# Kernel tuning notes

Hardware: AMD Instinct MI355X
Metric: run time of the kernel (lower is better)

## Reference

```python
import jax, jax.numpy as jnp
import numpy as np

N_NODES = 100000
N_EDGES = 1600000
NODE_DIM = 128
HIDDEN = 128
OUT_DIM = 128
N_GRAPHS = 64
LN_EPS = 1e-5


def setup_inputs() -> dict:
    key = jax.random.key(0)
    ks = jax.random.split(key, 14)

    def lin(k, fan_in, fan_out):
        bound = 1.0 / np.sqrt(fan_in)
        kw, kb = jax.random.split(k)
        W = jax.random.uniform(kw, (fan_in, fan_out), jnp.float32, -bound, bound)
        b = jax.random.uniform(kb, (fan_out,), jnp.float32, -bound, bound)
        return W, b

    node_features = jax.random.normal(ks[0], (N_NODES, NODE_DIM), jnp.float32)
    edge_index = jax.random.randint(ks[1], (2, N_EDGES), 0, N_NODES, jnp.int32)
    batch = jnp.sort(jax.random.randint(ks[2], (N_NODES,), 0, N_GRAPHS, jnp.int32))

    W1, b1 = lin(ks[3], NODE_DIM, HIDDEN)
    W2, b2 = lin(ks[4], HIDDEN, HIDDEN)
    W3, b3 = lin(ks[5], HIDDEN, OUT_DIM)
    Wm1, bm1 = lin(ks[6], OUT_DIM, HIDDEN)
    Wm2, bm2 = lin(ks[7], HIDDEN, OUT_DIM)
    ln_g = jnp.ones((OUT_DIM,), jnp.float32)
    ln_b = jnp.zeros((OUT_DIM,), jnp.float32)

    return dict(node_features=node_features, edge_index=edge_index, batch=batch,
                W1=W1, b1=b1, W2=W2, b2=b2, W3=W3, b3=b3,
                Wm1=Wm1, bm1=bm1, Wm2=Wm2, bm2=bm2, ln_g=ln_g, ln_b=ln_b)


def _gcn_precompute(edge_index, n_nodes):
    # Add self-loops; symmetric degree normalization (PyG GCNConv semantics).
    loops = jnp.arange(n_nodes, dtype=edge_index.dtype)
    src = jnp.concatenate([edge_index[0], loops])
    dst = jnp.concatenate([edge_index[1], loops])
    deg = jax.ops.segment_sum(jnp.ones_like(dst, jnp.float32), dst, num_segments=n_nodes)
    dinv = jax.lax.rsqrt(deg)  # deg >= 1 thanks to self-loops
    norm = dinv[src] * dinv[dst]  # [E + N]
    return src, dst, norm


def _gcn_layer(x, W, b, src, dst, norm, n_nodes):
    xw = x @ W                              # [N, F_out]
    msg = norm[:, None] * xw[src]           # [E+N, F_out] gather
    agg = jax.ops.segment_sum(msg, dst, num_segments=n_nodes)  # scatter-add
    return agg + b


def reference(node_features, edge_index, batch,
              W1, b1, W2, b2, W3, b3, Wm1, bm1, Wm2, bm2, ln_g, ln_b):
    n_nodes = node_features.shape[0]
    src, dst, norm = _gcn_precompute(edge_index, n_nodes)

    x = jax.nn.relu(_gcn_layer(node_features, W1, b1, src, dst, norm, n_nodes))
    x = jax.nn.relu(_gcn_layer(x, W2, b2, src, dst, norm, n_nodes))
    x = _gcn_layer(x, W3, b3, src, dst, norm, n_nodes)  # no relu on last layer

    # global mean pool per graph
    sums = jax.ops.segment_sum(x, batch, num_segments=N_GRAPHS)
    cnts = jax.ops.segment_sum(jnp.ones((n_nodes,), x.dtype), batch, num_segments=N_GRAPHS)
    g = sums / jnp.maximum(cnts, 1.0)[:, None]  # [G, OUT_DIM]

    # global reasoner MLP + LayerNorm
    h = jax.nn.relu(g @ Wm1 + bm1)
    y = h @ Wm2 + bm2
    mu = jnp.mean(y, axis=-1, keepdims=True)
    var = jnp.var(y, axis=-1, keepdims=True)
    y = (y - mu) * jax.lax.rsqrt(var + LN_EPS) * ln_g + ln_b
    return y
```

## Files before the change

### kernel.cpp

```cpp
#include <hip/hip_runtime.h>

#define FDIM 128
#define LN_EPS 1e-5f
#define NBKT_SHIFT 8
#define BKT_NODES 256
#define MAXBKT 512
#define CAP_SHIFT 13
#define BKT_CAP 8192

typedef short bf16x8 __attribute__((ext_vector_type(8)));
typedef float f32x4 __attribute__((ext_vector_type(4)));
typedef float f32x2 __attribute__((ext_vector_type(2)));
typedef ushort u16x8 __attribute__((ext_vector_type(8)));
typedef unsigned long long u64;
typedef long long i64;

static __device__ __forceinline__ ushort f2bf(float f) {
    union { float f; unsigned u; } v; v.f = f;
    unsigned r = v.u + 0x7FFFu + ((v.u >> 16) & 1u);
    return (ushort)(r >> 16);
}
static __device__ __forceinline__ float bf2f(ushort h) {
    union { unsigned u; float f; } v; v.u = ((unsigned)h) << 16;
    return v.f;
}
static __device__ __forceinline__ unsigned char f2fp8(float f) {
    return (unsigned char)__builtin_amdgcn_cvt_pk_fp8_f32(f, f, 0u, false);
}
static __device__ __forceinline__ float fp8tof(unsigned char b) {
    f32x2 p = __builtin_amdgcn_cvt_pk_f32_fp8((unsigned)b, false);
    return p[0];
}
static __device__ __forceinline__ void fp8x8_add(uint2 w, f32x2* acc) {
    acc[0] += __builtin_amdgcn_cvt_pk_f32_fp8(w.x, false);
    acc[1] += __builtin_amdgcn_cvt_pk_f32_fp8(w.x, true);
    acc[2] += __builtin_amdgcn_cvt_pk_f32_fp8(w.y, false);
    acc[3] += __builtin_amdgcn_cvt_pk_f32_fp8(w.y, true);
}


__launch_bounds__(256)
__global__ void k_bkt_scatter(const int* __restrict__ src, const int* __restrict__ dst,
                              int* __restrict__ bcur, unsigned* __restrict__ bktA,
                              int E, int nbkt) {
    __shared__ int h[2][MAXBKT], lbase[2][MAXBKT], lcur[2][MAXBKT];
    const int t = threadIdx.x;
    const int half = t >> 7;
    for (int i = t; i < 2 * MAXBKT; i += 256) ((int*)h)[i] = 0;
    __syncthreads();
    const int E4 = E >> 2;
    const int4* s4p = (const int4*)src;
    const int4* d4p = (const int4*)dst;
    int4 sv[4], dv[4]; bool ok[4];
#pragma unroll
    for (int r = 0; r < 4; r++) {
        int i4 = blockIdx.x * 1024 + r * 256 + t;
        ok[r] = (i4 < E4);
        if (ok[r]) {
            sv[r] = s4p[i4]; dv[r] = d4p[i4];
            atomicAdd(&h[half][dv[r].x >> NBKT_SHIFT], 1);
            atomicAdd(&h[half][dv[r].y >> NBKT_SHIFT], 1);
            atomicAdd(&h[half][dv[r].z >> NBKT_SHIFT], 1);
            atomicAdd(&h[half][dv[r].w >> NBKT_SHIFT], 1);
        }
    }
    __syncthreads();
    for (int i = t; i < 2 * nbkt; i += 256) {
        const int hh = (i >= nbkt) ? 1 : 0;
        const int b = hh ? (i - nbkt) : i;
        const int c = h[hh][b];
        lbase[hh][b] = c ? ((b << CAP_SHIFT) + atomicAdd(&bcur[b], c)) : 0;
        lcur[hh][b] = 0;
    }
    __syncthreads();
#pragma unroll
    for (int r = 0; r < 4; r++) {
        if (!ok[r]) continue;
        int ss[4] = {sv[r].x, sv[r].y, sv[r].z, sv[r].w};
        int dd[4] = {dv[r].x, dv[r].y, dv[r].z, dv[r].w};
#pragma unroll
        for (int j = 0; j < 4; j++) {
            int b = dd[j] >> NBKT_SHIFT;
            int p = atomicAdd(&lcur[half][b], 1);
            bktA[(size_t)lbase[half][b] + p] =
                ((unsigned)ss[j] << NBKT_SHIFT) | (unsigned)(dd[j] & (BKT_NODES - 1));
        }
    }
}


__launch_bounds__(512)
__global__ void k_build(const unsigned* __restrict__ bktA, const int* __restrict__ bcur,
                        int2* __restrict__ rowinfo, float* __restrict__ dinv,
                        int* __restrict__ csr_src, int N) {
    __shared__ int sorted[BKT_CAP];
    __shared__ int cnt[BKT_NODES];
    __shared__ int cur[BKT_NODES];
    __shared__ int wpart[4], wbase[4];
    const int t = threadIdx.x;
    const int b = blockIdx.x;
    const int nb = b << NBKT_SHIFT;
    if (t < BKT_NODES) cnt[t] = 0;
    __syncthreads();
    const int beg = b << CAP_SHIFT;
    const int tot = bcur[b];
    for (int i = t; i < tot; i += 512)
        atomicAdd(&cnt[bktA[beg + i] & (BKT_NODES - 1)], 1);
    __syncthreads();
    const int lane = t & 63, wv = t >> 6;
    int my = 0, x = 0;
    if (t < BKT_NODES) {
        my = cnt[t];
        x = my;
#pragma unroll
        for (int off = 1; off < 64; off <<= 1) {
            int y = __shfl_up(x, off, 64);
            if (lane >= off) x += y;
        }
        if (lane == 63) wpart[wv] = x;
    }
    __syncthreads();
    if (t == 0) {
        int s = 0;
        for (int w = 0; w < 4; w++) { int tmp = wpart[w]; wbase[w] = s; s += tmp; }
    }
    __syncthreads();
    if (t < BKT_NODES) {
        const int incl = x + wbase[wv];
        const int rbeg = incl - my;
        cur[t] = rbeg;
        const int n = nb + t;
        if (n < N) {
            rowinfo[n] = make_int2(beg + rbeg, my);
            dinv[n] = rsqrtf((float)(my + 1));
        }
    }
    __syncthreads();
    for (int i = t; i < tot; i += 512) {
        unsigned pr = bktA[beg + i];
        int d = pr & (BKT_NODES - 1);
        int p = atomicAdd(&cur[d], 1);
        sorted[p] = (int)(pr >> NBKT_SHIFT);
    }
    __syncthreads();
    for (int i = t; i < tot; i += 512)
        csr_src[beg + i] = sorted[i];
}


__global__ void k_prep_w(const float* __restrict__ Wa, const float* __restrict__ Wb,
                         const float* __restrict__ Wc, ushort* __restrict__ Wt_b,
                         unsigned char* __restrict__ Wt8, float* __restrict__ gsums,
                         int* __restrict__ bcur) {
    int idx = blockIdx.x * 256 + threadIdx.x;
    int layer = idx >> 14;
    int r = idx & 16383;
    int nn = r >> 7, kk = r & 127;
    if (layer == 0) {
        Wt_b[r] = f2bf(Wa[kk * 128 + nn]);
    } else {
        const float* W = (layer == 1) ? Wb : Wc;
        Wt8[(size_t)(layer - 1) * 16384 + r] = f2fp8(W[kk * 128 + nn]);
    }
    if (idx < 8192) gsums[idx] = 0.f;
    if (idx < MAXBKT) bcur[idx] = 0;
}


__launch_bounds__(256)
__global__ void k_gemm_f32(const float* __restrict__ X, const ushort* __restrict__ Wt,
                           const float* __restrict__ dinv, unsigned char* __restrict__ C,
                           int N) {
    __shared__ __align__(16) ushort As[128][136];
    __shared__ ushort Ws[128][136];
    const int t = threadIdx.x;
    const int row0 = blockIdx.x * 128;

#pragma unroll
    for (int i = 0; i < 8; i++) {
        int c = t + i * 256;
        int r = c >> 4, c8 = (c & 15) * 8;
        *(bf16x8*)&Ws[r][c8] = *(const bf16x8*)&Wt[r * 128 + c8];
    }
#pragma unroll
    for (int i = 0; i < 8; i++) {
        int c = t + i * 256;
        int r = c >> 4, c8 = (c & 15) * 8;
        int row = row0 + r;
        bf16x8 pk = {0, 0, 0, 0, 0, 0, 0, 0};
        if (row < N) {
            const float* sp = X + (size_t)row * FDIM + c8;
            float4 u0 = *(const float4*)(sp);
            float4 u1 = *(const float4*)(sp + 4);
            pk[0] = (short)f2bf(u0.x); pk[1] = (short)f2bf(u0.y);
            pk[2] = (short)f2bf(u0.z); pk[3] = (short)f2bf(u0.w);
            pk[4] = (short)f2bf(u1.x); pk[5] = (short)f2bf(u1.y);
            pk[6] = (short)f2bf(u1.z); pk[7] = (short)f2bf(u1.w);
        }
        *(bf16x8*)&As[r][c8] = pk;
    }
    __syncthreads();

    const int w = t >> 6, l = t & 63;
    const int m = l & 15, q = l >> 4;
    const int r0 = w * 32;

    bf16x8 a0[4], a1[4];
#pragma unroll
    for (int ks = 0; ks < 4; ks++) {
        a0[ks] = *(const bf16x8*)&As[r0 + m][ks * 32 + q * 8];
        a1[ks] = *(const bf16x8*)&As[r0 + 16 + m][ks * 32 + q * 8];
    }

    f32x4 acc0[8], acc1[8];
#pragma unroll
    for (int ct = 0; ct < 8; ct++) { acc0[ct] = {0, 0, 0, 0}; acc1[ct] = {0, 0, 0, 0}; }

#pragma unroll
    for (int ct = 0; ct < 8; ct++) {
#pragma unroll
        for (int ks = 0; ks < 4; ks++) {
            bf16x8 b = *(const bf16x8*)&Ws[ct * 16 + m][ks * 32 + q * 8];
            acc0[ct] = __builtin_amdgcn_mfma_f32_16x16x32_bf16(a0[ks], b, acc0[ct], 0, 0, 0);
            acc1[ct] = __builtin_amdgcn_mfma_f32_16x16x32_bf16(a1[ks], b, acc1[ct], 0, 0, 0);
        }
    }

    float dv0[4], dv1[4];
#pragma unroll
    for (int r = 0; r < 4; r++) {
        int row = row0 + r0 + q * 4 + r;
        dv0[r] = (row < N) ? dinv[row] : 0.f;
        dv1[r] = (row + 16 < N) ? dinv[row + 16] : 0.f;
    }

    __syncthreads();
    char* Ab = (char*)&As[0][0];
#pragma unroll
    for (int ct = 0; ct < 8; ct++) {
#pragma unroll
        for (int r = 0; r < 4; r++) {
            int rl = r0 + q * 4 + r;
            Ab[rl * 128 + ct * 16 + m] = (char)f2fp8(acc0[ct][r] * dv0[r]);
            Ab[(rl + 16) * 128 + ct * 16 + m] = (char)f2fp8(acc1[ct][r] * dv1[r]);
        }
    }
    __syncthreads();
    const uint4* As4 = (const uint4*)Ab;
#pragma unroll
    for (int i = 0; i < 4; i++) {
        int c = t + i * 256;
        int row = c >> 3;
        int col = (c & 7) * 16;
        int grow = row0 + row;
        if (grow < N) *(uint4*)&C[(size_t)grow * FDIM + col] = As4[c];
    }
}


__launch_bounds__(256)
__global__ void k_gemm_fp8(const unsigned char* __restrict__ X,
                           const unsigned char* __restrict__ W8,
                           const float* __restrict__ dinv, unsigned char* __restrict__ C,
                           int N) {
    __shared__ __align__(16) unsigned char As[128][144];
    __shared__ __align__(16) unsigned char Ws[128][144];
    const int t = threadIdx.x;
    const int row0 = blockIdx.x * 128;

#pragma unroll
    for (int i = 0; i < 4; i++) {
        int c = t + i * 256;
        int r = c >> 3, col = (c & 7) * 16;
        *(uint4*)&Ws[r][col] = *(const uint4*)&W8[r * 128 + col];
        int row = row0 + r;
        uint4 v = {0, 0, 0, 0};
        if (row < N) v = *(const uint4*)&X[(size_t)row * FDIM + col];
        *(uint4*)&As[r][col] = v;
    }
    __syncthreads();

    const int w = t >> 6, l = t & 63;
    const int m = l & 15, q = l >> 4;
    const int r0 = w * 32;

    i64 a0[4], a1[4];
#pragma unroll
    for (int ks = 0; ks < 4; ks++) {
        a0[ks] = *(const i64*)&As[r0 + m][ks * 32 + q * 8];
        a1[ks] = *(const i64*)&As[r0 + 16 + m][ks * 32 + q * 8];
    }

    f32x4 acc0[8], acc1[8];
#pragma unroll
    for (int ct = 0; ct < 8; ct++) { acc0[ct] = {0, 0, 0, 0}; acc1[ct] = {0, 0, 0, 0}; }

#pragma unroll
    for (int ct = 0; ct < 8; ct++) {
#pragma unroll
        for (int ks = 0; ks < 4; ks++) {
            i64 b = *(const i64*)&Ws[ct * 16 + m][ks * 32 + q * 8];
            acc0[ct] = __builtin_amdgcn_mfma_f32_16x16x32_fp8_fp8(a0[ks], b, acc0[ct], 0, 0, 0);
            acc1[ct] = __builtin_amdgcn_mfma_f32_16x16x32_fp8_fp8(a1[ks], b, acc1[ct], 0, 0, 0);
        }
    }

    float dv0[4], dv1[4];
#pragma unroll
    for (int r = 0; r < 4; r++) {
        int row = row0 + r0 + q * 4 + r;
        dv0[r] = (row < N) ? dinv[row] : 0.f;
        dv1[r] = (row + 16 < N) ? dinv[row + 16] : 0.f;
    }

    __syncthreads();
    char* Ab = (char*)&As[0][0];
#pragma unroll
    for (int ct = 0; ct < 8; ct++) {
#pragma unroll
        for (int r = 0; r < 4; r++) {
            int rl = r0 + q * 4 + r;
            Ab[rl * 128 + ct * 16 + m] = (char)f2fp8(acc0[ct][r] * dv0[r]);
            Ab[(rl + 16) * 128 + ct * 16 + m] = (char)f2fp8(acc1[ct][r] * dv1[r]);
        }
    }
    __syncthreads();
    const uint4* As4 = (const uint4*)Ab;
#pragma unroll
    for (int i = 0; i < 4; i++) {
        int c = t + i * 256;
        int row = c >> 3;
        int col = (c & 7) * 16;
        int grow = row0 + row;
        if (grow < N) *(uint4*)&C[(size_t)grow * FDIM + col] = As4[c];
    }
}


__launch_bounds__(256)
__global__ void k_aggregate(const unsigned char* __restrict__ xs8,
                            const int2* __restrict__ rowinfo,
                            const int* __restrict__ csr_src, const float* __restrict__ dinv,
                            const float* __restrict__ bias, unsigned char* __restrict__ out,
                            int N, int do_relu) {
    const int n = (blockIdx.x << 2) + (threadIdx.x >> 6);
    if (n >= N) return;
    const int l = threadIdx.x & 63;
    const int fl = l & 15;
    const int grp = l >> 4;
    const unsigned foff = (unsigned)fl << 3;

    f32x2 acc[4] = {{0, 0}, {0, 0}, {0, 0}, {0, 0}};
    if (grp == 0) {
        uint2 sv = *(const uint2*)(xs8 + (((unsigned)n << 7) | foff));
        fp8x8_add(sv, acc);
    }

    const int2 ri = rowinfo[n];
    const int beg = ri.x;
    const int deg = ri.y;

    for (int base = 0; base < deg; base += 64) {
        const int m = min(64, deg - base);
        int idx = 0;
        if (l < m) idx = csr_src[(unsigned)(beg + base + l)];
        int j = grp;
        if (j < m) {
            int s0 = __shfl(idx, j, 64);
            uint2 v0 = *(const uint2*)(xs8 + (((unsigned)s0 << 7) | foff));
            int j2 = j + 4;
            if (j2 < m) {
                int s1 = __shfl(idx, j2, 64);
                uint2 v1 = *(const uint2*)(xs8 + (((unsigned)s1 << 7) | foff));
                for (j = j2 + 4; j < m; j += 4) {
                    int s2 = __shfl(idx, j, 64);
                    uint2 v2 = *(const uint2*)(xs8 + (((unsigned)s2 << 7) | foff));
                    fp8x8_add(v0, acc);
                    v0 = v1; v1 = v2;
                }
                fp8x8_add(v0, acc);
                fp8x8_add(v1, acc);
            } else {
                fp8x8_add(v0, acc);
            }
        }
    }

    float a[8] = {acc[0][0], acc[0][1], acc[1][0], acc[1][1],
                  acc[2][0], acc[2][1], acc[3][0], acc[3][1]};
#pragma unroll
    for (int k = 0; k < 8; k++) {
        a[k] += __shfl_xor(a[k], 16, 64);
        a[k] += __shfl_xor(a[k], 32, 64);
    }

    if (grp == 0) {
        const float d = dinv[n];
        const float4 b0 = ((const float4*)bias)[fl * 2];
        const float4 b1 = ((const float4*)bias)[fl * 2 + 1];
        const float bb[8] = {b0.x, b0.y, b0.z, b0.w, b1.x, b1.y, b1.z, b1.w};
        float v[8];
#pragma unroll
        for (int k = 0; k < 8; k++) {
            v[k] = d * a[k] + bb[k];
            if (do_relu) v[k] = fmaxf(v[k], 0.f);
        }
        uint2 o;
        unsigned d0 = __builtin_amdgcn_cvt_pk_fp8_f32(v[0], v[1], 0u, false);
        o.x = __builtin_amdgcn_cvt_pk_fp8_f32(v[2], v[3], d0, true);
        unsigned d1 = __builtin_amdgcn_cvt_pk_fp8_f32(v[4], v[5], 0u, false);
        o.y = __builtin_amdgcn_cvt_pk_fp8_f32(v[6], v[7], d1, true);
        ((uint2*)out)[(size_t)n * 16 + fl] = o;
    }
}


__launch_bounds__(256)
__global__ void k_pool(const unsigned char* __restrict__ x3, const int* __restrict__ batch,
                       float* __restrict__ sums, int N) {
    const int t = threadIdx.x;
    const int fq = t & 31;
    const int sub = t >> 5;
    const int n0 = blockIdx.x * 256 + sub * 32;
    if (n0 >= N) return;
    const int n1 = (n0 + 32 < N) ? n0 + 32 : N;

    f32x4 acc = {0.f, 0.f, 0.f, 0.f};
    int cur = batch[n0];
    for (int n = n0; n < n1; n++) {
        int g = batch[n];
        if (g != cur) {
            float* s = &sums[cur * FDIM + (fq << 2)];
            atomicAdd(s + 0, acc[0]); atomicAdd(s + 1, acc[1]);
            atomicAdd(s + 2, acc[2]); atomicAdd(s + 3, acc[3]);
            acc = (f32x4){0.f, 0.f, 0.f, 0.f};
            cur = g;
        }
        unsigned w = *(const unsigned*)(x3 + ((size_t)n << 7) + (fq << 2));
        f32x2 lo = __builtin_amdgcn_cvt_pk_f32_fp8(w, false);
        f32x2 hi = __builtin_amdgcn_cvt_pk_f32_fp8(w, true);
        acc[0] += lo[0]; acc[1] += lo[1]; acc[2] += hi[0]; acc[3] += hi[1];
    }
    float* s = &sums[cur * FDIM + (fq << 2)];
    atomicAdd(s + 0, acc[0]); atomicAdd(s + 1, acc[1]);
    atomicAdd(s + 2, acc[2]); atomicAdd(s + 3, acc[3]);
}


__launch_bounds__(128)
__global__ void k_final(const float* __restrict__ sums, const int* __restrict__ batch, int N,
                        const float* __restrict__ Wm1, const float* __restrict__ bm1,
                        const float* __restrict__ Wm2, const float* __restrict__ bm2,
                        const float* __restrict__ ln_g, const float* __restrict__ ln_b,
                        float* __restrict__ out) {
    const int g = blockIdx.x;
    const int t = threadIdx.x;

    int lo = 0, hi = N;
    while (lo < hi) { int mid = (lo + hi) >> 1; if (batch[mid] < g) lo = mid + 1; else hi = mid; }
    int lo2 = lo, hi2 = N;
    while (lo2 < hi2) { int mid = (lo2 + hi2) >> 1; if (batch[mid] < g + 1) lo2 = mid + 1; else hi2 = mid; }
    float cnt = (float)(lo2 - lo);

    float gl = sums[g * FDIM + t] / fmaxf(cnt, 1.0f);

    __shared__ float gbuf[FDIM];
    __shared__ float hbuf[FDIM];
    __shared__ float wsum[4];
    gbuf[t] = gl;
    __syncthreads();

    float h = bm1[t];
#pragma unroll 8
    for (int k = 0; k < FDIM; k++) h += gbuf[k] * Wm1[k * FDIM + t];
    h = fmaxf(h, 0.f);
    hbuf[t] = h;
    __syncthreads();

    float y = bm2[t];
#pragma unroll 8
    for (int k = 0; k < FDIM; k++) y += hbuf[k] * Wm2[k * FDIM + t];

    float s = y, s2 = y * y;
#pragma unroll
    for (int off = 32; off > 0; off >>= 1) {
        s += __shfl_down(s, off, 64);
        s2 += __shfl_down(s2, off, 64);
    }
    if ((t & 63) == 0) { wsum[t >> 6] = s; wsum[2 + (t >> 6)] = s2; }
    __syncthreads();
    float sum = wsum[0] + wsum[1];
    float sumsq = wsum[2] + wsum[3];
    float mu = sum * (1.0f / FDIM);
    float var = sumsq * (1.0f / FDIM) - mu * mu;
    float r = rsqrtf(var + LN_EPS);
    out[g * FDIM + t] = (y - mu) * r * ln_g[t] + ln_b[t];
}


extern "C" void kernel_launch(void* const* d_in, const int* in_sizes, int n_in,
                              void* d_out, int out_size, void* d_ws, size_t ws_size,
                              hipStream_t stream) {
    const float* x_in  = (const float*)d_in[0];
    const int*   eidx  = (const int*)d_in[1];
    const int*   batch = (const int*)d_in[2];
    const float* W1 = (const float*)d_in[3];
    const float* b1 = (const float*)d_in[4];
    const float* W2 = (const float*)d_in[5];
    const float* b2 = (const float*)d_in[6];
    const float* W3 = (const float*)d_in[7];
    const float* b3 = (const float*)d_in[8];
    const float* Wm1 = (const float*)d_in[9];
    const float* bm1 = (const float*)d_in[10];
    const float* Wm2 = (const float*)d_in[11];
    const float* bm2 = (const float*)d_in[12];
    const float* ln_g = (const float*)d_in[13];
    const float* ln_b = (const float*)d_in[14];
    float* out = (float*)d_out;

    const int N = in_sizes[0] / FDIM;
    const int E = in_sizes[1] / 2;
    const int G = out_size / FDIM;

    const int* src = eidx;
    const int* dst = eidx + E;

    const int nbkt = (N + BKT_NODES - 1) >> NBKT_SHIFT;

    char* p = (char*)d_ws;
    unsigned* bktA = (unsigned*)p;    p += (size_t)nbkt * BKT_CAP * 4;
    unsigned char* B0q = (unsigned char*)p; p += (size_t)N * FDIM;
    unsigned char* B1q = (unsigned char*)p; p += (size_t)N * FDIM;
    int* csr_src = (int*)p;           p += (size_t)nbkt * BKT_CAP * 4;
    int2* rowinfo = (int2*)p;         p += (size_t)N * 8;
    float* dinv = (float*)p;          p += (size_t)N * 4;
    ushort* Wt_b = (ushort*)p;        p += 16384 * 2;
    unsigned char* Wt8 = (unsigned char*)p; p += 2 * 16384;
    float* gsums = (float*)p;         p += (size_t)G * FDIM * 4;
    int* bcur = (int*)p;              p += MAXBKT * 4;

    const int TPB = 256;
    dim3 blk(TPB);
    dim3 gAgg((N + 3) / 4);
    dim3 gTile((N + 127) / 128);
    const int nEb = (E + 4095) / 4096;

    k_prep_w<<<dim3(192), blk, 0, stream>>>(W1, W2, W3, Wt_b, Wt8, gsums, bcur);
    k_bkt_scatter<<<dim3(nEb), blk, 0, stream>>>(src, dst, bcur, bktA, E, nbkt);
    k_build<<<dim3(nbkt), dim3(512), 0, stream>>>(bktA, bcur, rowinfo, dinv, csr_src, N);

    k_gemm_f32<<<gTile, blk, 0, stream>>>(x_in, Wt_b, dinv, B0q, N);
    k_aggregate<<<gAgg, blk, 0, stream>>>(B0q, rowinfo, csr_src, dinv, b1, B1q, N, 1);

    k_gemm_fp8<<<gTile, blk, 0, stream>>>(B1q, Wt8, dinv, B0q, N);
    k_aggregate<<<gAgg, blk, 0, stream>>>(B0q, rowinfo, csr_src, dinv, b2, B1q, N, 1);

    k_gemm_fp8<<<gTile, blk, 0, stream>>>(B1q, Wt8 + 16384, dinv, B0q, N);
    k_aggregate<<<gAgg, blk, 0, stream>>>(B0q, rowinfo, csr_src, dinv, b3, B1q, N, 0);

    k_pool<<<dim3((N + 255) / 256), blk, 0, stream>>>(B1q, batch, gsums, N);
    k_final<<<dim3(G), dim3(FDIM), 0, stream>>>(gsums, batch, N, Wm1, bm1, Wm2, bm2,
                                                ln_g, ln_b, out);
}
```

Baseline: 384.4 us.

## Use half-wave per node in aggregation and fuse mean-pool into last layer

The aggregation kernel now assigns 32 lanes per node (8 nodes per block) instead of 64, with a deeper three-stage gather pipeline and a single cross-lane reduction. The final layer's aggregation accumulates pooled sums directly, via shared-memory atomics when a block's nodes share one graph and global atomics otherwise, which removes the separate pool kernel and the fp8 write and re-read of the last layer's output. The cost is more work per lane for high-degree nodes and global atomic contention in blocks that span a graph boundary. Pooling also now sums values before fp8 rounding, which slightly changes the numerics.

```diff
diff --git a/kernel.cpp b/kernel.cpp
--- a/kernel.cpp
+++ b/kernel.cpp
@@ -342,44 +342,68 @@
                             const int2* __restrict__ rowinfo,
                             const int* __restrict__ csr_src, const float* __restrict__ dinv,
                             const float* __restrict__ bias, unsigned char* __restrict__ out,
-                            int N, int do_relu) {
-    const int n = (blockIdx.x << 2) + (threadIdx.x >> 6);
-    if (n >= N) return;
-    const int l = threadIdx.x & 63;
-    const int fl = l & 15;
-    const int grp = l >> 4;
+                            const int* __restrict__ batch, float* __restrict__ gsums,
+                            int N, int do_relu, int fuse_pool) {
+    __shared__ float gsum_s[FDIM];
+    __shared__ int gb_s[8];
+    const int t = threadIdx.x;
+    const int l = t & 63;
+    const int node_slot = t >> 5;
+    const int n = blockIdx.x * 8 + node_slot;
+    const bool active = (n < N);
+    const int hl = l & 31;
+    const int fl = hl & 15;
+    const int grp = hl >> 4;
+    const int selbase = l & 32;
     const unsigned foff = (unsigned)fl << 3;
 
+    if (fuse_pool) {
+        if (t < FDIM) gsum_s[t] = 0.f;
+        if (t < 8) {
+            int nn = blockIdx.x * 8 + t;
+            gb_s[t] = batch[nn < N ? nn : (N - 1)];
+        }
+        __syncthreads();
+    }
+
     f32x2 acc[4] = {{0, 0}, {0, 0}, {0, 0}, {0, 0}};
-    if (grp == 0) {
+    int2 ri = active ? rowinfo[n] : make_int2(0, 0);
+    if (active && grp == 0) {
         uint2 sv = *(const uint2*)(xs8 + (((unsigned)n << 7) | foff));
         fp8x8_add(sv, acc);
     }
-
-    const int2 ri = rowinfo[n];
     const int beg = ri.x;
     const int deg = ri.y;
 
-    for (int base = 0; base < deg; base += 64) {
-        const int m = min(64, deg - base);
+    for (int base = 0; base < deg; base += 32) {
+        const int m = min(32, deg - base);
         int idx = 0;
-        if (l < m) idx = csr_src[(unsigned)(beg + base + l)];
+        if (hl < m) idx = csr_src[(unsigned)(beg + base + hl)];
         int j = grp;
         if (j < m) {
-            int s0 = __shfl(idx, j, 64);
+            int s0 = __shfl(idx, selbase | j, 64);
             uint2 v0 = *(const uint2*)(xs8 + (((unsigned)s0 << 7) | foff));
-            int j2 = j + 4;
-            if (j2 < m) {
-                int s1 = __shfl(idx, j2, 64);
+            int j1 = j + 2;
+            if (j1 < m) {
+                int s1 = __shfl(idx, selbase | j1, 64);
                 uint2 v1 = *(const uint2*)(xs8 + (((unsigned)s1 << 7) | foff));
-                for (j = j2 + 4; j < m; j += 4) {
-                    int s2 = __shfl(idx, j, 64);
+                int j2 = j1 + 2;
+                if (j2 < m) {
+                    int s2 = __shfl(idx, selbase | j2, 64);
                     uint2 v2 = *(const uint2*)(xs8 + (((unsigned)s2 << 7) | foff));
+                    for (j = j2 + 2; j < m; j += 2) {
+                        int s3 = __shfl(idx, selbase | j, 64);
+                        uint2 v3 = *(const uint2*)(xs8 + (((unsigned)s3 << 7) | foff));
+                        fp8x8_add(v0, acc);
+                        v0 = v1; v1 = v2; v2 = v3;
+                    }
                     fp8x8_add(v0, acc);
-                    v0 = v1; v1 = v2;
+                    fp8x8_add(v1, acc);
+                    fp8x8_add(v2, acc);
+                } else {
+                    fp8x8_add(v0, acc);
+                    fp8x8_add(v1, acc);
                 }
-                fp8x8_add(v0, acc);
-                fp8x8_add(v1, acc);
             } else {
                 fp8x8_add(v0, acc);
             }
@@ -389,12 +413,9 @@
     float a[8] = {acc[0][0], acc[0][1], acc[1][0], acc[1][1],
                   acc[2][0], acc[2][1], acc[3][0], acc[3][1]};
 #pragma unroll
-    for (int k = 0; k < 8; k++) {
-        a[k] += __shfl_xor(a[k], 16, 64);
-        a[k] += __shfl_xor(a[k], 32, 64);
-    }
-
-    if (grp == 0) {
+    for (int k = 0; k < 8; k++) a[k] += __shfl_xor(a[k], 16, 64);
+
+    if (active && grp == 0) {
         const float d = dinv[n];
         const float4 b0 = ((const float4*)bias)[fl * 2];
         const float4 b1 = ((const float4*)bias)[fl * 2 + 1];
@@ -405,45 +426,31 @@
             v[k] = d * a[k] + bb[k];
             if (do_relu) v[k] = fmaxf(v[k], 0.f);
         }
-        uint2 o;
-        unsigned d0 = __builtin_amdgcn_cvt_pk_fp8_f32(v[0], v[1], 0u, false);
-        o.x = __builtin_amdgcn_cvt_pk_fp8_f32(v[2], v[3], d0, true);
-        unsigned d1 = __builtin_amdgcn_cvt_pk_fp8_f32(v[4], v[5], 0u, false);
-        o.y = __builtin_amdgcn_cvt_pk_fp8_f32(v[6], v[7], d1, true);
-        ((uint2*)out)[(size_t)n * 16 + fl] = o;
-    }
-}
-
-
-__launch_bounds__(256)
-__global__ void k_pool(const unsigned char* __restrict__ x3, const int* __restrict__ batch,
-                       float* __restrict__ sums, int N) {
-    const int t = threadIdx.x;
-    const int fq = t & 31;
-    const int sub = t >> 5;
-    const int n0 = blockIdx.x * 256 + sub * 32;
-    if (n0 >= N) return;
-    const int n1 = (n0 + 32 < N) ? n0 + 32 : N;
-
-    f32x4 acc = {0.f, 0.f, 0.f, 0.f};
-    int cur = batch[n0];
-    for (int n = n0; n < n1; n++) {
-        int g = batch[n];
-        if (g != cur) {
-            float* s = &sums[cur * FDIM + (fq << 2)];
-            atomicAdd(s + 0, acc[0]); atomicAdd(s + 1, acc[1]);
-            atomicAdd(s + 2, acc[2]); atomicAdd(s + 3, acc[3]);
-            acc = (f32x4){0.f, 0.f, 0.f, 0.f};
-            cur = g;
-        }
-        unsigned w = *(const unsigned*)(x3 + ((size_t)n << 7) + (fq << 2));
-        f32x2 lo = __builtin_amdgcn_cvt_pk_f32_fp8(w, false);
-        f32x2 hi = __builtin_amdgcn_cvt_pk_f32_fp8(w, true);
-        acc[0] += lo[0]; acc[1] += lo[1]; acc[2] += hi[0]; acc[3] += hi[1];
-    }
-    float* s = &sums[cur * FDIM + (fq << 2)];
-    atomicAdd(s + 0, acc[0]); atomicAdd(s + 1, acc[1]);
-    atomicAdd(s + 2, acc[2]); atomicAdd(s + 3, acc[3]);
+        if (!fuse_pool) {
+            uint2 o;
+            unsigned d0 = __builtin_amdgcn_cvt_pk_fp8_f32(v[0], v[1], 0u, false);
+            o.x = __builtin_amdgcn_cvt_pk_fp8_f32(v[2], v[3], d0, true);
+            unsigned d1 = __builtin_amdgcn_cvt_pk_fp8_f32(v[4], v[5], 0u, false);
+            o.y = __builtin_amdgcn_cvt_pk_fp8_f32(v[6], v[7], d1, true);
+            ((uint2*)out)[(size_t)n * 16 + fl] = o;
+        } else {
+            const bool uni = (gb_s[0] == gb_s[7]);
+            if (uni) {
+#pragma unroll
+                for (int k = 0; k < 8; k++) atomicAdd(&gsum_s[foff + k], v[k]);
+            } else {
+                const int g = gb_s[node_slot];
+#pragma unroll
+                for (int k = 0; k < 8; k++) atomicAdd(&gsums[g * FDIM + foff + k], v[k]);
+            }
+        }
+    }
+    if (fuse_pool) {
+        __syncthreads();
+        if (gb_s[0] == gb_s[7]) {
+            if (t < FDIM) atomicAdd(&gsums[gb_s[0] * FDIM + t], gsum_s[t]);
+        }
+    }
 }
 
 
@@ -541,7 +548,7 @@
 
     const int TPB = 256;
     dim3 blk(TPB);
-    dim3 gAgg((N + 3) / 4);
+    dim3 gAgg((N + 7) / 8);
     dim3 gTile((N + 127) / 128);
     const int nEb = (E + 4095) / 4096;
 
@@ -550,15 +557,17 @@
     k_build<<<dim3(nbkt), dim3(512), 0, stream>>>(bktA, bcur, rowinfo, dinv, csr_src, N);
 
     k_gemm_f32<<<gTile, blk, 0, stream>>>(x_in, Wt_b, dinv, B0q, N);
-    k_aggregate<<<gAgg, blk, 0, stream>>>(B0q, rowinfo, csr_src, dinv, b1, B1q, N, 1);
+    k_aggregate<<<gAgg, blk, 0, stream>>>(B0q, rowinfo, csr_src, dinv, b1, B1q,
+                                          batch, gsums, N, 1, 0);
 
     k_gemm_fp8<<<gTile, blk, 0, stream>>>(B1q, Wt8, dinv, B0q, N);
-    k_aggregate<<<gAgg, blk, 0, stream>>>(B0q, rowinfo, csr_src, dinv, b2, B1q, N, 1);
+    k_aggregate<<<gAgg, blk, 0, stream>>>(B0q, rowinfo, csr_src, dinv, b2, B1q,
+                                          batch, gsums, N, 1, 0);
 
     k_gemm_fp8<<<gTile, blk, 0, stream>>>(B1q, Wt8 + 16384, dinv, B0q, N);
-    k_aggregate<<<gAgg, blk, 0, stream>>>(B0q, rowinfo, csr_src, dinv, b3, B1q, N, 0);
-
-    k_pool<<<dim3((N + 255) / 256), blk, 0, stream>>>(B1q, batch, gsums, N);
+    k_aggregate<<<gAgg, blk, 0, stream>>>(B0q, rowinfo, csr_src, dinv, b3, B1q,
+                                          batch, gsums, N, 0, 1);
+
     k_final<<<dim3(G), dim3(FDIM), 0, stream>>>(gsums, batch, N, Wm1, bm1, Wm2, bm2,
                                                 ln_g, ln_b, out);
 }
```

New measurement: 388.5 us. About the same (+1.1%).
